# Kernel optimization log

Measured on AMD Instinct MI355X. Metric: run time of the kernel, lower is better.

## Reference

```python
import math
import jax, jax.numpy as jnp
import numpy as np

D_MODEL = 768
D_CROSS = 768
D_HEAD = 64
N_HEADS = D_MODEL // D_HEAD  # 12
D_FF = D_MODEL * 3           # 2304
EPS = 1e-6
N_FREQ = D_HEAD // 8         # freqs per axis (3 axes -> theta dim 24, rotates first 48 of 64 dims)


def make_rope_freqs():
    # k-diffusion style geometric frequencies in [pi, 10*pi), one table shared per head
    n = N_HEADS * N_FREQ
    f = np.exp(np.linspace(math.log(math.pi), math.log(10.0 * math.pi), n + 1)[:-1])
    return jnp.asarray(f.reshape(N_FREQ, N_HEADS).T, dtype=jnp.float32)  # [nh, N_FREQ]

ROPE_FREQS = make_rope_freqs()


def rms_norm(x, scale):
    ms = jnp.mean(jnp.square(x), axis=-1, keepdims=True)
    return x * (scale * jax.lax.rsqrt(ms + EPS))


def cos_scale(q, k, scale):
    # cosine-sim QK rescale: unit-normalize q,k per head then multiply by sqrt(learned scale)
    s = jnp.sqrt(scale)[:, None, None]  # [nh,1,1]
    q = q * (s * jax.lax.rsqrt(jnp.sum(jnp.square(q), -1, keepdims=True) + EPS))
    k = k * (s * jax.lax.rsqrt(jnp.sum(jnp.square(k), -1, keepdims=True) + EPS))
    return q, k


def rope_theta(pos):
    # pos [b,l,3] -> theta [b,nh,l,3*N_FREQ]
    b, l, _ = pos.shape
    th = pos[..., None, :, None] * ROPE_FREQS[:, None, :]  # [b,l,nh,3,N_FREQ]
    th = th.reshape(b, l, N_HEADS, 3 * N_FREQ)
    return jnp.swapaxes(th, 1, 2)  # movedim(-2,-3)


def apply_rope(x, theta):
    d = theta.shape[-1]
    x1, x2, x3 = x[..., :d], x[..., d:2 * d], x[..., 2 * d:]
    c, s = jnp.cos(theta), jnp.sin(theta)
    return jnp.concatenate([x1 * c - x2 * s, x2 * c + x1 * s, x3], axis=-1)


def sdpa(q, k, v):
    # scale=1.0 (cosine-sim already scaled)
    a = jax.nn.softmax(jnp.einsum('bhqe,bhke->bhqk', q, k), axis=-1)
    return jnp.einsum('bhqk,bhke->bhqe', a, v)


def reference(x, pos, x_cross, pos_cross,
              sa_norm_scale, sa_wqkv, sa_scale, sa_wout,
              ca_norm_scale, ca_norm_cross_scale, ca_wq, ca_wkv, ca_scale, ca_wout,
              ff_norm_scale, ff_wup, ff_wdown):
    b, l, _ = x.shape
    lc = x_cross.shape[1]

    # --- self attention ---
    h = rms_norm(x, sa_norm_scale)
    qkv = (h @ sa_wqkv.T).reshape(b, l, 3, N_HEADS, D_HEAD).transpose(2, 0, 3, 1, 4)
    q, k, v = qkv[0], qkv[1], qkv[2]  # [b,nh,l,e]
    q, k = cos_scale(q, k, sa_scale)
    theta = rope_theta(pos)
    q = apply_rope(q, theta)
    k = apply_rope(k, theta)
    o = sdpa(q, k, v)
    o = jnp.swapaxes(o, 1, 2).reshape(b, l, D_MODEL)
    x = o @ sa_wout.T + x

    # --- cross attention ---
    h = rms_norm(x, ca_norm_scale)
    hc = rms_norm(x_cross, ca_norm_cross_scale)
    q = (h @ ca_wq.T).reshape(b, l, N_HEADS, D_HEAD).transpose(0, 2, 1, 3)
    kv = (hc @ ca_wkv.T).reshape(b, lc, 2, N_HEADS, D_HEAD).transpose(2, 0, 3, 1, 4)
    k, v = kv[0], kv[1]
    q, k = cos_scale(q, k, ca_scale)
    q = apply_rope(q, rope_theta(pos))
    k = apply_rope(k, rope_theta(pos_cross))
    o = sdpa(q, k, v)
    o = jnp.swapaxes(o, 1, 2).reshape(b, l, D_MODEL)
    x = o @ ca_wout.T + x

    # --- SwiGLU FFN ---
    u = rms_norm(x, ff_norm_scale) @ ff_wup.T  # [b,l,2*d_ff]
    a, g = jnp.split(u, 2, axis=-1)
    x = (a * jax.nn.silu(g)) @ ff_wdown.T + x
    return x


def setup_inputs() -> dict:
    key = jax.random.key(0)
    ks = jax.random.split(key, 16)
    B, L = 2, 2048

    def w(k, out_f, in_f):
        return jax.random.normal(k, (out_f, in_f), dtype=jnp.float32) * (1.0 / math.sqrt(in_f))

    return {
        'x': jax.random.normal(ks[0], (B, L, D_MODEL), dtype=jnp.float32),
        'pos': jax.random.uniform(ks[1], (B, L, 3), dtype=jnp.float32),
        'x_cross': jax.random.normal(ks[2], (B, L, D_CROSS), dtype=jnp.float32),
        'pos_cross': jax.random.uniform(ks[3], (B, L, 3), dtype=jnp.float32),
        'sa_norm_scale': jnp.ones((D_MODEL,), jnp.float32),
        'sa_wqkv': w(ks[4], 3 * D_MODEL, D_MODEL),
        'sa_scale': jnp.full((N_HEADS,), 10.0, jnp.float32),
        'sa_wout': w(ks[5], D_MODEL, D_MODEL) * 0.02,
        'ca_norm_scale': jnp.ones((D_MODEL,), jnp.float32),
        'ca_norm_cross_scale': jnp.ones((D_CROSS,), jnp.float32),
        'ca_wq': w(ks[6], D_MODEL, D_MODEL),
        'ca_wkv': w(ks[7], 2 * D_MODEL, D_CROSS),
        'ca_scale': jnp.full((N_HEADS,), 10.0, jnp.float32),
        'ca_wout': w(ks[8], D_MODEL, D_MODEL) * 0.02,
        'ff_norm_scale': jnp.ones((D_MODEL,), jnp.float32),
        'ff_wup': w(ks[9], 2 * D_FF, D_MODEL),
        'ff_wdown': w(ks[10], D_MODEL, D_FF) * 0.02,
    }
```

## Files before the change

kernel.cpp:

```cpp
#include <hip/hip_runtime.h>
#include <hip/hip_bf16.h>
#include <math.h>

typedef __hip_bfloat16 bf16;

#define B 2
#define L 2048
#define DM 768
#define NH 12
#define DH 64
#define DFF 2304
#define M_TOK (B * L)

typedef __attribute__((ext_vector_type(8))) short bfrag;
typedef __attribute__((ext_vector_type(4))) float ffrag;
typedef __attribute__((ext_vector_type(16))) float facc16;

__device__ __forceinline__ float waveSum(float v) {
#pragma unroll
  for (int o = 32; o > 0; o >>= 1) v += __shfl_down(v, o, 64);
  return v;
}

__device__ __forceinline__ void gld16(void* l, const void* g) {
  __builtin_amdgcn_global_load_lds((const __attribute__((address_space(1))) unsigned*)g,
                                   (__attribute__((address_space(3))) unsigned*)l, 16, 0, 0);
}

#define ASW(row, chunk) (((row) << 6) + ((((chunk) ^ ((row)&7))) << 3))

__global__ void k_castall(const float* __restrict__ s0, const float* __restrict__ s1,
                          const float* __restrict__ s2, const float* __restrict__ s3,
                          const float* __restrict__ s4, const float* __restrict__ s5,
                          const float* __restrict__ s6, bf16* __restrict__ dst) {
  const size_t DM2 = (size_t)DM * DM;
  size_t u = ((size_t)blockIdx.x * 256 + threadIdx.x) * 4;
  if (u >= 17 * DM2) return;
  const float* src;
  size_t loc;
  if (u < 3 * DM2) { src = s0; loc = u; }
  else if (u < 4 * DM2) { src = s1; loc = u - 3 * DM2; }
  else if (u < 5 * DM2) { src = s2; loc = u - 4 * DM2; }
  else if (u < 7 * DM2) { src = s3; loc = u - 5 * DM2; }
  else if (u < 8 * DM2) { src = s4; loc = u - 7 * DM2; }
  else if (u < 14 * DM2) { src = s5; loc = u - 8 * DM2; }
  else { src = s6; loc = u - 14 * DM2; }
  float4 v = *(const float4*)&src[loc];
  bf16* d = dst + u;
  d[0] = __float2bfloat16(v.x);
  d[1] = __float2bfloat16(v.y);
  d[2] = __float2bfloat16(v.z);
  d[3] = __float2bfloat16(v.w);
}

__global__ __launch_bounds__(256) void k_rmsnorm(const float* __restrict__ in,
                                                 const float* __restrict__ scale,
                                                 bf16* __restrict__ out) {
  int row = blockIdx.x;
  int t = threadIdx.x;
  const float* r = in + (size_t)row * DM;
  float x0 = r[t], x1 = r[t + 256], x2 = r[t + 512];
  float ss = x0 * x0 + x1 * x1 + x2 * x2;
  ss = waveSum(ss);
  __shared__ float red[4];
  int w = t >> 6, ln = t & 63;
  if (ln == 0) red[w] = ss;
  __syncthreads();
  float tot = red[0] + red[1] + red[2] + red[3];
  float g = rsqrtf(tot / (float)DM + 1e-6f);
  bf16* o = out + (size_t)row * DM;
  o[t] = __float2bfloat16(x0 * g * scale[t]);
  o[t + 256] = __float2bfloat16(x1 * g * scale[t + 256]);
  o[t + 512] = __float2bfloat16(x2 * g * scale[t + 512]);
}

template <int NT, int OBF>
__global__ __launch_bounds__(256) void k_gemm(const bf16* __restrict__ A,
                                              const bf16* __restrict__ W,
                                              float* __restrict__ C,
                                              bf16* __restrict__ Cb,
                                              const float* __restrict__ res,
                                              int M, int N, int K) {
  __shared__ __align__(16) bf16 As[128 * 32];
  __shared__ __align__(16) bf16 Bs[NT * 32];
  const int t = threadIdx.x;
  const int w = t >> 6, lane = t & 63;
  const int m0 = blockIdx.y * 128, n0 = blockIdx.x * NT;
  const int quad = lane >> 4, l16 = lane & 15;
  constexpr int MI = (NT == 128) ? 4 : 2;
  const int wrow = (NT == 128) ? (w >> 1) * 64 : w * 32;
  const int wcol = (NT == 128) ? (w & 1) * 64 : 0;

  ffrag acc[MI][4];
#pragma unroll
  for (int i = 0; i < MI; i++)
#pragma unroll
    for (int j = 0; j < 4; j++) acc[i][j] = (ffrag){0.f, 0.f, 0.f, 0.f};

  for (int k0 = 0; k0 < K; k0 += 32) {
#pragma unroll
    for (int it = 0; it < 2; it++) {
      int lc = (w * 2 + it) * 64 + lane;
      int row = lc >> 2;
      int kc = (lc & 3) ^ ((row >> 1) & 3);
      gld16(&As[lc * 8], &A[(size_t)(m0 + row) * K + k0 + kc * 8]);
    }
    if (NT == 128) {
#pragma unroll
      for (int it = 0; it < 2; it++) {
        int lc = (w * 2 + it) * 64 + lane;
        int row = lc >> 2;
        int kc = (lc & 3) ^ ((row >> 1) & 3);
        gld16(&Bs[lc * 8], &W[(size_t)(n0 + row) * K + k0 + kc * 8]);
      }
    } else {
      int lc = w * 64 + lane;
      int row = lc >> 2;
      int kc = (lc & 3) ^ ((row >> 1) & 3);
      gld16(&Bs[lc * 8], &W[(size_t)(n0 + row) * K + k0 + kc * 8]);
    }
    __syncthreads();
    bfrag af[MI], bfv[4];
#pragma unroll
    for (int i = 0; i < MI; i++) {
      int r = wrow + i * 16 + l16;
      af[i] = *(const bfrag*)&As[r * 32 + (quad ^ ((r >> 1) & 3)) * 8];
    }
#pragma unroll
    for (int j = 0; j < 4; j++) {
      int r = wcol + j * 16 + l16;
      bfv[j] = *(const bfrag*)&Bs[r * 32 + (quad ^ ((r >> 1) & 3)) * 8];
    }
#pragma unroll
    for (int i = 0; i < MI; i++)
#pragma unroll
      for (int j = 0; j < 4; j++)
        acc[i][j] = __builtin_amdgcn_mfma_f32_16x16x32_bf16(af[i], bfv[j], acc[i][j], 0, 0, 0);
    __syncthreads();
  }
#pragma unroll
  for (int i = 0; i < MI; i++) {
    int mrow = m0 + wrow + i * 16 + quad * 4;
#pragma unroll
    for (int j = 0; j < 4; j++) {
      int ncol = n0 + wcol + j * 16 + l16;
#pragma unroll
      for (int r = 0; r < 4; r++) {
        float v = acc[i][j][r];
        size_t idx = (size_t)(mrow + r) * N + ncol;
        if (OBF) {
          Cb[idx] = __float2bfloat16(v);
        } else {
          if (res) v += res[idx];
          C[idx] = v;
        }
      }
    }
  }
}

__global__ __launch_bounds__(256) void k_ffup(const bf16* __restrict__ A,
                                              const bf16* __restrict__ Wup,
                                              bf16* __restrict__ Out) {
  __shared__ __align__(16) bf16 As[128 * 32];
  __shared__ __align__(16) bf16 Ba[64 * 32];
  __shared__ __align__(16) bf16 Bg[64 * 32];
  const int t = threadIdx.x, w = t >> 6, lane = t & 63;
  const int m0 = blockIdx.y * 128, n0 = blockIdx.x * 64;
  const int quad = lane >> 4, l16 = lane & 15;

  ffrag aa[2][4], ag[2][4];
#pragma unroll
  for (int i = 0; i < 2; i++)
#pragma unroll
    for (int j = 0; j < 4; j++) {
      aa[i][j] = (ffrag){0.f, 0.f, 0.f, 0.f};
      ag[i][j] = (ffrag){0.f, 0.f, 0.f, 0.f};
    }

  for (int k0 = 0; k0 < DM; k0 += 32) {
#pragma unroll
    for (int it = 0; it < 2; it++) {
      int lc = (w * 2 + it) * 64 + lane;
      int row = lc >> 2;
      int kc = (lc & 3) ^ ((row >> 1) & 3);
      gld16(&As[lc * 8], &A[(size_t)(m0 + row) * DM + k0 + kc * 8]);
    }
    {
      int lc = w * 64 + lane;
      int row = lc >> 2;
      int kc = (lc & 3) ^ ((row >> 1) & 3);
      gld16(&Ba[lc * 8], &Wup[(size_t)(n0 + row) * DM + k0 + kc * 8]);
      gld16(&Bg[lc * 8], &Wup[(size_t)(DFF + n0 + row) * DM + k0 + kc * 8]);
    }
    __syncthreads();
    bfrag af[2], ba[4], bg[4];
#pragma unroll
    for (int i = 0; i < 2; i++) {
      int r = w * 32 + i * 16 + l16;
      af[i] = *(const bfrag*)&As[r * 32 + (quad ^ ((r >> 1) & 3)) * 8];
    }
#pragma unroll
    for (int j = 0; j < 4; j++) {
      int r = j * 16 + l16;
      int sw = (quad ^ ((r >> 1) & 3)) * 8;
      ba[j] = *(const bfrag*)&Ba[r * 32 + sw];
      bg[j] = *(const bfrag*)&Bg[r * 32 + sw];
    }
#pragma unroll
    for (int i = 0; i < 2; i++)
#pragma unroll
      for (int j = 0; j < 4; j++) {
        aa[i][j] = __builtin_amdgcn_mfma_f32_16x16x32_bf16(af[i], ba[j], aa[i][j], 0, 0, 0);
        ag[i][j] = __builtin_amdgcn_mfma_f32_16x16x32_bf16(af[i], bg[j], ag[i][j], 0, 0, 0);
      }
    __syncthreads();
  }
#pragma unroll
  for (int i = 0; i < 2; i++) {
    int mrow = m0 + w * 32 + i * 16 + quad * 4;
#pragma unroll
    for (int j = 0; j < 4; j++) {
      int ncol = n0 + j * 16 + l16;
#pragma unroll
      for (int r = 0; r < 4; r++) {
        float a = aa[i][j][r], g = ag[i][j][r];
        float v = a * g / (1.f + __expf(-g));
        Out[(size_t)(mrow + r) * DFF + ncol] = __float2bfloat16(v);
      }
    }
  }
}

__device__ __forceinline__ float rope_apply(float x, const float* __restrict__ pos3, float s,
                                            int h, int lane) {
  float ss = x * x;
#pragma unroll
  for (int m = 32; m > 0; m >>= 1) ss += __shfl_xor(ss, m, 64);
  x *= s * rsqrtf(ss + 1e-6f);
  int j = lane < 24 ? lane : (lane < 48 ? lane - 24 : 0);
  int partner = lane < 24 ? lane + 24 : (lane < 48 ? lane - 24 : lane);
  float other = __shfl(x, partner, 64);
  if (lane < 48) {
    int c = j >> 3, f = j & 7;
    float fr = __expf(1.14472988584940017f +
                      (float)(f * 12 + h) * (2.30258509299404568f / 96.0f));
    float th = pos3[c] * fr;
    float st, ct;
    sincosf(th, &st, &ct);
    return (lane < 24) ? (x * ct - other * st) : (x * ct + other * st);
  }
  return x;
}

__global__ __launch_bounds__(256) void k_ropeqk(const bf16* __restrict__ inQ, int strQ, int offQ,
                                                const bf16* __restrict__ inK, int strK, int offK,
                                                const float* __restrict__ posQ,
                                                const float* __restrict__ posK,
                                                const float* __restrict__ scale,
                                                bf16* __restrict__ outQ, bf16* __restrict__ outK) {
  int item = blockIdx.x * 4 + (threadIdx.x >> 6);
  int lane = threadIdx.x & 63;
  int l = item % L;
  int bh = item / L;
  int h = bh % NH;
  int b = bh / NH;
  float s = sqrtf(scale[h]);
  size_t tokrow = (size_t)(b * L + l);
  float xq = __bfloat162float(inQ[tokrow * strQ + offQ + h * DH + lane]);
  float oq = rope_apply(xq, &posQ[tokrow * 3], s, h, lane);
  outQ[(size_t)item * DH + lane] = __float2bfloat16(oq);
  float xk = __bfloat162float(inK[tokrow * strK + offK + h * DH + lane]);
  float ok = rope_apply(xk, &posK[tokrow * 3], s, h, lane);
  outK[(size_t)item * DH + lane] = __float2bfloat16(ok);
}

__global__ __launch_bounds__(256) void k_vtrans(const bf16* __restrict__ in, int stride, int off,
                                                bf16* __restrict__ Vt) {
  __shared__ __align__(16) bf16 St[64 * 64];
  int lt = blockIdx.x & 31, bh = blockIdx.x >> 5;
  int h = bh % NH, b = bh / NH;
  int t = threadIdx.x;
#pragma unroll
  for (int pass = 0; pass < 2; pass++) {
    int cid = t + pass * 256;
    int r = cid >> 3, c = cid & 7;
    *(float4*)&St[ASW(r, c)] =
        *(const float4*)&in[(size_t)(b * L + lt * 64 + r) * stride + off + h * DH + c * 8];
  }
  __syncthreads();
  const short* Ss = (const short*)St;
#pragma unroll
  for (int pass = 0; pass < 2; pass++) {
    int cid = t + pass * 256;
    int d = cid >> 3, oc = cid & 7;
    bfrag tmp;
#pragma unroll
    for (int i = 0; i < 8; i++) {
      int tok = oc * 8 + i;
      tmp[i] = Ss[(tok << 6) + ((((d >> 3) ^ (tok & 7))) << 3) + (d & 7)];
    }
    *(bfrag*)&Vt[((size_t)bh * DH + d) * L + lt * 64 + oc * 8] = tmp;
  }
}

__global__ __launch_bounds__(256) void k_attn_mfma(const bf16* __restrict__ Q,
                                                   const bf16* __restrict__ K,
                                                   const bf16* __restrict__ Vt,
                                                   const float* __restrict__ scale,
                                                   bf16* __restrict__ O) {
  __shared__ __align__(16) char smem[24576 + 512];
  bf16* Ks = (bf16*)smem;
  bf16* Vs = (bf16*)(smem + 8192);
  bf16* Ps = (bf16*)(smem + 16384);
  float* Oex = (float*)smem;
  float* Lred = (float*)(smem + 24576);
  int qt = blockIdx.x & 31, bh = blockIdx.x >> 5;
  int h = bh % NH, b = bh / NH;
  float smax = scale[h];
  int t = threadIdx.x, w = t >> 6, lane = t & 63;
  int hh = lane >> 5, l32 = lane & 31;
  int qsub = w >> 1, ksub = w & 1;
  int sr = t >> 3, sc = t & 7;

  const bf16* kbase = K + (size_t)(bh * L) * DH;
  const bf16* vbase = Vt + (size_t)bh * DH * L;

  const bf16* qrow = Q + ((size_t)(bh * L) + qt * 64 + qsub * 32 + l32) * DH;
  bfrag qf[4];
#pragma unroll
  for (int c = 0; c < 4; c++) qf[c] = *(const bfrag*)&qrow[c * 16 + hh * 8];

  facc16 o0, o1;
#pragma unroll
  for (int i = 0; i < 16; i++) { o0[i] = 0.f; o1[i] = 0.f; }
  float l_run = 0.f;
  int qg = qsub * 32 + l32;

  for (int kt = 0; kt < 32; kt++) {
    int k0 = kt * 64;
    __syncthreads();
#pragma unroll
    for (int half = 0; half < 2; half++) {
      int r = sr + half * 32;
      *(float4*)&Ks[ASW(r, sc)] = *(const float4*)&kbase[(size_t)(k0 + r) * DH + sc * 8];
      *(float4*)&Vs[ASW(r, sc)] = *(const float4*)&vbase[(size_t)r * L + k0 + sc * 8];
    }
    __syncthreads();
    facc16 s;
#pragma unroll
    for (int i = 0; i < 16; i++) s[i] = 0.f;
#pragma unroll
    for (int c = 0; c < 4; c++) {
      bfrag kf = *(const bfrag*)&Ks[ASW(ksub * 32 + l32, c * 2 + hh)];
      s = __builtin_amdgcn_mfma_f32_32x32x16_bf16(kf, qf[c], s, 0, 0, 0);
    }
#pragma unroll
    for (int reg = 0; reg < 16; reg++) {
      float p = __expf(s[reg] - smax);
      l_run += p;
      int keyg = ksub * 32 + (reg & 3) + 8 * (reg >> 2) + 4 * hh;
      Ps[(qg << 6) + ((((keyg >> 3) ^ (qg & 7))) << 3) + (keyg & 7)] = __float2bfloat16(p);
    }
    bfrag pf0 = *(const bfrag*)&Ps[ASW(qg, ksub * 4 + hh)];
    bfrag pf1 = *(const bfrag*)&Ps[ASW(qg, ksub * 4 + 2 + hh)];
    {
      bfrag vf;
      vf = *(const bfrag*)&Vs[ASW(l32, ksub * 4 + hh)];
      o0 = __builtin_amdgcn_mfma_f32_32x32x16_bf16(pf0, vf, o0, 0, 0, 0);
      vf = *(const bfrag*)&Vs[ASW(l32, ksub * 4 + 2 + hh)];
      o0 = __builtin_amdgcn_mfma_f32_32x32x16_bf16(pf1, vf, o0, 0, 0, 0);
      vf = *(const bfrag*)&Vs[ASW(32 + l32, ksub * 4 + hh)];
      o1 = __builtin_amdgcn_mfma_f32_32x32x16_bf16(pf0, vf, o1, 0, 0, 0);
      vf = *(const bfrag*)&Vs[ASW(32 + l32, ksub * 4 + 2 + hh)];
      o1 = __builtin_amdgcn_mfma_f32_32x32x16_bf16(pf1, vf, o1, 0, 0, 0);
    }
  }
  l_run += __shfl_xor(l_run, 32, 64);
  __syncthreads();
  {
    int gd = (ksub ^ 1) * 32 + l32;
#pragma unroll
    for (int reg = 0; reg < 16; reg++) {
      int row = (reg & 3) + 8 * (reg >> 2) + 4 * hh;
      float gv = ksub ? o0[reg] : o1[reg];
      Oex[(size_t)(qsub * 32 + row) * 64 + gd] = gv;
    }
  }
  if (lane < 32) Lred[ksub * 64 + qsub * 32 + lane] = l_run;
  __syncthreads();
  {
    int d = ksub * 32 + l32;
#pragma unroll
    for (int reg = 0; reg < 16; reg++) {
      int row = (reg & 3) + 8 * (reg >> 2) + 4 * hh;
      int qg2 = qsub * 32 + row;
      float ltot = Lred[qg2] + Lred[64 + qg2];
      float keep = ksub ? o1[reg] : o0[reg];
      float v = (keep + Oex[(size_t)qg2 * 64 + d]) / ltot;
      O[(((size_t)(b * L) + qt * 64 + qg2) * NH + h) * DH + d] = __float2bfloat16(v);
    }
  }
}

extern "C" void kernel_launch(void* const* d_in, const int* in_sizes, int n_in,
                              void* d_out, int out_size, void* d_ws, size_t ws_size,
                              hipStream_t stream) {
  const float* x = (const float*)d_in[0];
  const float* pos = (const float*)d_in[1];
  const float* x_cross = (const float*)d_in[2];
  const float* pos_cross = (const float*)d_in[3];
  const float* sa_norm_scale = (const float*)d_in[4];
  const float* sa_wqkv = (const float*)d_in[5];
  const float* sa_scale = (const float*)d_in[6];
  const float* sa_wout = (const float*)d_in[7];
  const float* ca_norm_scale = (const float*)d_in[8];
  const float* ca_norm_cross_scale = (const float*)d_in[9];
  const float* ca_wq = (const float*)d_in[10];
  const float* ca_wkv = (const float*)d_in[11];
  const float* ca_scale = (const float*)d_in[12];
  const float* ca_wout = (const float*)d_in[13];
  const float* ff_norm_scale = (const float*)d_in[14];
  const float* ff_wup = (const float*)d_in[15];
  const float* ff_wdown = (const float*)d_in[16];
  float* out = (float*)d_out;

  float* ws = (float*)d_ws;
  const size_t S = (size_t)M_TOK * DM;
  float* xbuf = ws;
  bf16* b16 = (bf16*)(ws + S);
  bf16* qkvb = b16;
  bf16* qb = b16 + 3 * S;
  bf16* kb = b16 + 4 * S;
  bf16* vtb = b16 + 5 * S;
  bf16* hb = b16 + 6 * S;
  bf16* hcb = b16 + 7 * S;
  bf16* obb = b16 + 8 * S;
  bf16* wqkvb = b16 + 9 * S;
  bf16* woutb = wqkvb + (size_t)3 * DM * DM;
  bf16* wqb = woutb + (size_t)DM * DM;
  bf16* wkvb = wqb + (size_t)DM * DM;
  bf16* wout2b = wkvb + (size_t)2 * DM * DM;
  bf16* wupb = wout2b + (size_t)DM * DM;
  bf16* wdownb = wupb + (size_t)2 * DFF * DM;
  bf16* ffb = qkvb;

  const int ropeGrid = B * NH * L / 4;
  const int attnGrid = B * NH * (L / 64);
  const int vtGrid = B * NH * (L / 64);
  const size_t DM2 = (size_t)DM * DM;
  const int castGrid = (int)((17 * DM2 / 4 + 255) / 256);

  k_castall<<<castGrid, 256, 0, stream>>>(sa_wqkv, sa_wout, ca_wq, ca_wkv, ca_wout, ff_wup,
                                          ff_wdown, wqkvb);

  k_rmsnorm<<<M_TOK, 256, 0, stream>>>(x_cross, ca_norm_cross_scale, hcb);

  k_rmsnorm<<<M_TOK, 256, 0, stream>>>(x, sa_norm_scale, hb);
  k_gemm<128, 1><<<dim3(3 * DM / 128, M_TOK / 128), 256, 0, stream>>>(
      hb, wqkvb, nullptr, qkvb, nullptr, M_TOK, 3 * DM, DM);
  k_ropeqk<<<ropeGrid, 256, 0, stream>>>(qkvb, 3 * DM, 0, qkvb, 3 * DM, DM, pos, pos, sa_scale,
                                         qb, kb);
  k_vtrans<<<vtGrid, 256, 0, stream>>>(qkvb, 3 * DM, 2 * DM, vtb);
  k_attn_mfma<<<attnGrid, 256, 0, stream>>>(qb, kb, vtb, sa_scale, obb);
  k_gemm<64, 0><<<dim3(DM / 64, M_TOK / 128), 256, 0, stream>>>(
      obb, woutb, xbuf, nullptr, x, M_TOK, DM, DM);

  k_rmsnorm<<<M_TOK, 256, 0, stream>>>(xbuf, ca_norm_scale, hb);
  k_gemm<64, 1><<<dim3(DM / 64, M_TOK / 128), 256, 0, stream>>>(
      hb, wqb, nullptr, qkvb, nullptr, M_TOK, DM, DM);
  k_gemm<128, 1><<<dim3(2 * DM / 128, M_TOK / 128), 256, 0, stream>>>(
      hcb, wkvb, nullptr, qkvb + S, nullptr, M_TOK, 2 * DM, DM);
  k_ropeqk<<<ropeGrid, 256, 0, stream>>>(qkvb, DM, 0, qkvb + S, 2 * DM, 0, pos, pos_cross,
                                         ca_scale, qb, kb);
  k_vtrans<<<vtGrid, 256, 0, stream>>>(qkvb + S, 2 * DM, DM, vtb);
  k_attn_mfma<<<attnGrid, 256, 0, stream>>>(qb, kb, vtb, ca_scale, obb);
  k_gemm<64, 0><<<dim3(DM / 64, M_TOK / 128), 256, 0, stream>>>(
      obb, wout2b, xbuf, nullptr, xbuf, M_TOK, DM, DM);

  k_rmsnorm<<<M_TOK, 256, 0, stream>>>(xbuf, ff_norm_scale, hb);
  k_ffup<<<dim3(DFF / 64, M_TOK / 128), 256, 0, stream>>>(hb, wupb, ffb);
  k_gemm<64, 0><<<dim3(DM / 64, M_TOK / 128), 256, 0, stream>>>(
      ffb, wdownb, out, nullptr, xbuf, M_TOK, DM, DFF);
}
```

Baseline: 490.0 us.

## Double-buffer LDS tiles in GEMM, FF-up and attention loops

The GEMM, fused FF-up and attention kernels now keep two LDS buffers per operand. The next K or KV tile is prefetched into the idle buffer while MFMAs run on the current one, so each iteration needs one barrier instead of two. The attention K/V staging also moves from register float4 copies to the direct global-to-LDS helper, with an equivalent swizzle. The cost is doubled shared memory, about 41KB per attention block, which may reduce occupancy, and correctness depends on the async loads having completed before the barrier.

```diff
diff --git a/kernel.cpp b/kernel.cpp
--- a/kernel.cpp
+++ b/kernel.cpp
@@ -81,8 +81,8 @@
                                               bf16* __restrict__ Cb,
                                               const float* __restrict__ res,
                                               int M, int N, int K) {
-  __shared__ __align__(16) bf16 As[128 * 32];
-  __shared__ __align__(16) bf16 Bs[NT * 32];
+  __shared__ __align__(16) bf16 As[2 * 128 * 32];
+  __shared__ __align__(16) bf16 Bs[2 * NT * 32];
   const int t = threadIdx.x;
   const int w = t >> 6, lane = t & 63;
   const int m0 = blockIdx.y * 128, n0 = blockIdx.x * NT;
@@ -97,13 +97,13 @@
 #pragma unroll
     for (int j = 0; j < 4; j++) acc[i][j] = (ffrag){0.f, 0.f, 0.f, 0.f};
 
-  for (int k0 = 0; k0 < K; k0 += 32) {
+  auto stage = [&](int k0, int sel) {
 #pragma unroll
     for (int it = 0; it < 2; it++) {
       int lc = (w * 2 + it) * 64 + lane;
       int row = lc >> 2;
       int kc = (lc & 3) ^ ((row >> 1) & 3);
-      gld16(&As[lc * 8], &A[(size_t)(m0 + row) * K + k0 + kc * 8]);
+      gld16(&As[sel * 4096 + lc * 8], &A[(size_t)(m0 + row) * K + k0 + kc * 8]);
     }
     if (NT == 128) {
 #pragma unroll
@@ -111,32 +111,40 @@
         int lc = (w * 2 + it) * 64 + lane;
         int row = lc >> 2;
         int kc = (lc & 3) ^ ((row >> 1) & 3);
-        gld16(&Bs[lc * 8], &W[(size_t)(n0 + row) * K + k0 + kc * 8]);
+        gld16(&Bs[sel * 4096 + lc * 8], &W[(size_t)(n0 + row) * K + k0 + kc * 8]);
       }
     } else {
       int lc = w * 64 + lane;
       int row = lc >> 2;
       int kc = (lc & 3) ^ ((row >> 1) & 3);
-      gld16(&Bs[lc * 8], &W[(size_t)(n0 + row) * K + k0 + kc * 8]);
-    }
+      gld16(&Bs[sel * 2048 + lc * 8], &W[(size_t)(n0 + row) * K + k0 + kc * 8]);
+    }
+  };
+
+  const int NK = K >> 5;
+  stage(0, 0);
+  for (int kt = 0; kt < NK; kt++) {
+    int cur = kt & 1;
     __syncthreads();
+    if (kt + 1 < NK) stage((kt + 1) * 32, cur ^ 1);
+    const bf16* Ab = As + cur * 4096;
+    const bf16* Bb = Bs + cur * (NT == 128 ? 4096 : 2048);
     bfrag af[MI], bfv[4];
 #pragma unroll
     for (int i = 0; i < MI; i++) {
       int r = wrow + i * 16 + l16;
-      af[i] = *(const bfrag*)&As[r * 32 + (quad ^ ((r >> 1) & 3)) * 8];
+      af[i] = *(const bfrag*)&Ab[r * 32 + (quad ^ ((r >> 1) & 3)) * 8];
     }
 #pragma unroll
     for (int j = 0; j < 4; j++) {
       int r = wcol + j * 16 + l16;
-      bfv[j] = *(const bfrag*)&Bs[r * 32 + (quad ^ ((r >> 1) & 3)) * 8];
+      bfv[j] = *(const bfrag*)&Bb[r * 32 + (quad ^ ((r >> 1) & 3)) * 8];
     }
 #pragma unroll
     for (int i = 0; i < MI; i++)
 #pragma unroll
       for (int j = 0; j < 4; j++)
         acc[i][j] = __builtin_amdgcn_mfma_f32_16x16x32_bf16(af[i], bfv[j], acc[i][j], 0, 0, 0);
-    __syncthreads();
   }
 #pragma unroll
   for (int i = 0; i < MI; i++) {
@@ -162,9 +170,9 @@
 __global__ __launch_bounds__(256) void k_ffup(const bf16* __restrict__ A,
                                               const bf16* __restrict__ Wup,
                                               bf16* __restrict__ Out) {
-  __shared__ __align__(16) bf16 As[128 * 32];
-  __shared__ __align__(16) bf16 Ba[64 * 32];
-  __shared__ __align__(16) bf16 Bg[64 * 32];
+  __shared__ __align__(16) bf16 As[2 * 128 * 32];
+  __shared__ __align__(16) bf16 Ba[2 * 64 * 32];
+  __shared__ __align__(16) bf16 Bg[2 * 64 * 32];
   const int t = threadIdx.x, w = t >> 6, lane = t & 63;
   const int m0 = blockIdx.y * 128, n0 = blockIdx.x * 64;
   const int quad = lane >> 4, l16 = lane & 15;
@@ -178,34 +186,44 @@
       ag[i][j] = (ffrag){0.f, 0.f, 0.f, 0.f};
     }
 
-  for (int k0 = 0; k0 < DM; k0 += 32) {
+  auto stage = [&](int k0, int sel) {
 #pragma unroll
     for (int it = 0; it < 2; it++) {
       int lc = (w * 2 + it) * 64 + lane;
       int row = lc >> 2;
       int kc = (lc & 3) ^ ((row >> 1) & 3);
-      gld16(&As[lc * 8], &A[(size_t)(m0 + row) * DM + k0 + kc * 8]);
+      gld16(&As[sel * 4096 + lc * 8], &A[(size_t)(m0 + row) * DM + k0 + kc * 8]);
     }
     {
       int lc = w * 64 + lane;
       int row = lc >> 2;
       int kc = (lc & 3) ^ ((row >> 1) & 3);
-      gld16(&Ba[lc * 8], &Wup[(size_t)(n0 + row) * DM + k0 + kc * 8]);
-      gld16(&Bg[lc * 8], &Wup[(size_t)(DFF + n0 + row) * DM + k0 + kc * 8]);
-    }
+      gld16(&Ba[sel * 2048 + lc * 8], &Wup[(size_t)(n0 + row) * DM + k0 + kc * 8]);
+      gld16(&Bg[sel * 2048 + lc * 8], &Wup[(size_t)(DFF + n0 + row) * DM + k0 + kc * 8]);
+    }
+  };
+
+  const int NK = DM / 32;
+  stage(0, 0);
+  for (int kt = 0; kt < NK; kt++) {
+    int cur = kt & 1;
     __syncthreads();
+    if (kt + 1 < NK) stage((kt + 1) * 32, cur ^ 1);
+    const bf16* Ab = As + cur * 4096;
+    const bf16* Bab = Ba + cur * 2048;
+    const bf16* Bgb = Bg + cur * 2048;
     bfrag af[2], ba[4], bg[4];
 #pragma unroll
     for (int i = 0; i < 2; i++) {
       int r = w * 32 + i * 16 + l16;
-      af[i] = *(const bfrag*)&As[r * 32 + (quad ^ ((r >> 1) & 3)) * 8];
+      af[i] = *(const bfrag*)&Ab[r * 32 + (quad ^ ((r >> 1) & 3)) * 8];
     }
 #pragma unroll
     for (int j = 0; j < 4; j++) {
       int r = j * 16 + l16;
       int sw = (quad ^ ((r >> 1) & 3)) * 8;
-      ba[j] = *(const bfrag*)&Ba[r * 32 + sw];
-      bg[j] = *(const bfrag*)&Bg[r * 32 + sw];
+      ba[j] = *(const bfrag*)&Bab[r * 32 + sw];
+      bg[j] = *(const bfrag*)&Bgb[r * 32 + sw];
     }
 #pragma unroll
     for (int i = 0; i < 2; i++)
@@ -214,7 +232,6 @@
         aa[i][j] = __builtin_amdgcn_mfma_f32_16x16x32_bf16(af[i], ba[j], aa[i][j], 0, 0, 0);
         ag[i][j] = __builtin_amdgcn_mfma_f32_16x16x32_bf16(af[i], bg[j], ag[i][j], 0, 0, 0);
       }
-    __syncthreads();
   }
 #pragma unroll
   for (int i = 0; i < 2; i++) {
@@ -309,19 +326,18 @@
                                                    const bf16* __restrict__ Vt,
                                                    const float* __restrict__ scale,
                                                    bf16* __restrict__ O) {
-  __shared__ __align__(16) char smem[24576 + 512];
+  __shared__ __align__(16) char smem[40960 + 512];
   bf16* Ks = (bf16*)smem;
-  bf16* Vs = (bf16*)(smem + 8192);
-  bf16* Ps = (bf16*)(smem + 16384);
+  bf16* Vs = (bf16*)(smem + 16384);
+  bf16* Ps = (bf16*)(smem + 32768);
   float* Oex = (float*)smem;
-  float* Lred = (float*)(smem + 24576);
+  float* Lred = (float*)(smem + 40960);
   int qt = blockIdx.x & 31, bh = blockIdx.x >> 5;
   int h = bh % NH, b = bh / NH;
   float smax = scale[h];
   int t = threadIdx.x, w = t >> 6, lane = t & 63;
   int hh = lane >> 5, l32 = lane & 31;
   int qsub = w >> 1, ksub = w & 1;
-  int sr = t >> 3, sc = t & 7;
 
   const bf16* kbase = K + (size_t)(bh * L) * DH;
   const bf16* vbase = Vt + (size_t)bh * DH * L;
@@ -337,22 +353,33 @@
   float l_run = 0.f;
   int qg = qsub * 32 + l32;
 
+  auto stageKV = [&](int kt, int sel) {
+    int k0 = kt * 64;
+    bf16* Kb = Ks + sel * 4096;
+    bf16* Vb = Vs + sel * 4096;
+#pragma unroll
+    for (int h2 = 0; h2 < 2; h2++) {
+      int r = w * 8 + (lane >> 3) + h2 * 32;
+      int kc = (lane & 7) ^ (r & 7);
+      int ldsrow = (w * 8 + h2 * 32) * 64;
+      gld16(&Kb[ldsrow + lane * 8], &kbase[(size_t)(k0 + r) * DH + kc * 8]);
+      gld16(&Vb[ldsrow + lane * 8], &vbase[(size_t)r * L + k0 + kc * 8]);
+    }
+  };
+
+  stageKV(0, 0);
   for (int kt = 0; kt < 32; kt++) {
-    int k0 = kt * 64;
+    int cur = kt & 1;
     __syncthreads();
-#pragma unroll
-    for (int half = 0; half < 2; half++) {
-      int r = sr + half * 32;
-      *(float4*)&Ks[ASW(r, sc)] = *(const float4*)&kbase[(size_t)(k0 + r) * DH + sc * 8];
-      *(float4*)&Vs[ASW(r, sc)] = *(const float4*)&vbase[(size_t)r * L + k0 + sc * 8];
-    }
-    __syncthreads();
+    if (kt < 31) stageKV(kt + 1, cur ^ 1);
+    const bf16* Kb = Ks + cur * 4096;
+    const bf16* Vb = Vs + cur * 4096;
     facc16 s;
 #pragma unroll
     for (int i = 0; i < 16; i++) s[i] = 0.f;
 #pragma unroll
     for (int c = 0; c < 4; c++) {
-      bfrag kf = *(const bfrag*)&Ks[ASW(ksub * 32 + l32, c * 2 + hh)];
+      bfrag kf = *(const bfrag*)&Kb[ASW(ksub * 32 + l32, c * 2 + hh)];
       s = __builtin_amdgcn_mfma_f32_32x32x16_bf16(kf, qf[c], s, 0, 0, 0);
     }
 #pragma unroll
@@ -366,13 +393,13 @@
     bfrag pf1 = *(const bfrag*)&Ps[ASW(qg, ksub * 4 + 2 + hh)];
     {
       bfrag vf;
-      vf = *(const bfrag*)&Vs[ASW(l32, ksub * 4 + hh)];
+      vf = *(const bfrag*)&Vb[ASW(l32, ksub * 4 + hh)];
       o0 = __builtin_amdgcn_mfma_f32_32x32x16_bf16(pf0, vf, o0, 0, 0, 0);
-      vf = *(const bfrag*)&Vs[ASW(l32, ksub * 4 + 2 + hh)];
+      vf = *(const bfrag*)&Vb[ASW(l32, ksub * 4 + 2 + hh)];
       o0 = __builtin_amdgcn_mfma_f32_32x32x16_bf16(pf1, vf, o0, 0, 0, 0);
-      vf = *(const bfrag*)&Vs[ASW(32 + l32, ksub * 4 + hh)];
+      vf = *(const bfrag*)&Vb[ASW(32 + l32, ksub * 4 + hh)];
       o1 = __builtin_amdgcn_mfma_f32_32x32x16_bf16(pf0, vf, o1, 0, 0, 0);
-      vf = *(const bfrag*)&Vs[ASW(32 + l32, ksub * 4 + 2 + hh)];
+      vf = *(const bfrag*)&Vb[ASW(32 + l32, ksub * 4 + 2 + hh)];
       o1 = __builtin_amdgcn_mfma_f32_32x32x16_bf16(pf1, vf, o1, 0, 0, 0);
     }
   }
```

New measurement: 485.5 us. No clear change (-0.9%).
